# Kernel tuning notes

Measured on AMD Instinct MI355X. Metric: run time of the kernel, lower is better.

Reference implementation:

```python
import jax, jax.numpy as jnp
import numpy as np

N = 8192
D = 512
N_SLICE = 64
K = 8
H = 30 * K  # 240


def _gen_k_slice(rng):
    xx = rng.normal(0.0, 1.0, (N_SLICE, K, D))
    slices = np.zeros((N_SLICE, K, D), dtype=np.float64)
    for i in range(N_SLICE):
        _, _, vh = np.linalg.svd(xx[i], full_matrices=False)
        slices[i] = vh
    return slices.astype(np.float32)


def setup_inputs() -> dict:
    key = jax.random.key(0)
    k1, k2, k3, k4, k5, k6, k7 = jax.random.split(key, 7)
    rng = np.random.default_rng(0)
    # conv weights: PyTorch Conv1d default init ~ U(-s, s), s = 1/sqrt(fan_in)
    s1 = 1.0 / np.sqrt(K)
    s3 = 1.0 / np.sqrt(H)
    return {
        "X": jax.random.normal(k1, (N, D), dtype=jnp.float32),
        "Y": jax.random.normal(k2, (N, D), dtype=jnp.float32),
        "X_noise": jax.random.normal(k3, (N, N_SLICE * K), dtype=jnp.float32),
        "thetas": jnp.asarray(_gen_k_slice(rng)),                     # [S, K, D]
        "W1": jax.random.uniform(k4, (N_SLICE, H, K), jnp.float32, -s1, s1),
        "b1": jax.random.uniform(k5, (N_SLICE, H), jnp.float32, -s1, s1),
        "W3": jax.random.uniform(k6, (N_SLICE, H), jnp.float32, -s3, s3),
        "b3": jax.random.uniform(k7, (N_SLICE,), jnp.float32, -s3, s3),
        "sigma_noise": 0,
    }


def _mlp(sample, W1, b1, W3, b3):
    # sample: [N, S, K] -> grouped 1x1 conv k->H, relu, grouped conv H->1
    h1 = jax.nn.relu(jnp.einsum('nsk,shk->nsh', sample, W1) + b1[None])
    return jnp.einsum('nsh,sh->ns', h1, W3) + b3[None]  # [N, S]


def reference(X, Y, X_noise, thetas, W1, b1, W3, b3, sigma_noise):
    # batched per-slice projections (fuses the n_slice matmul loop)
    x_sample = jnp.einsum('nd,skd->nsk', X, thetas)  # [N, S, K]
    y_sample = jnp.einsum('nd,skd->nsk', Y, thetas)
    if sigma_noise > 0:
        x_sample = x_sample + sigma_noise * X_noise.reshape(X.shape[0], N_SLICE, K)
    pred_x = _mlp(x_sample, W1, b1, W3, b3)  # [N, S]
    pred_y = _mlp(y_sample, W1, b1, W3, b3)
    n_y = pred_y.shape[0]
    ret = jnp.mean(pred_x, axis=0) - jax.nn.logsumexp(
        pred_y - jnp.log(jnp.float32(n_y)), axis=0)
    return jnp.mean(-ret)
```

## Files before the change

kernel.cpp:

```cpp
#include <hip/hip_runtime.h>
#include <hip/hip_bf16.h>

#define NROWS 8192
#define DDIM  512
#define NS    64
#define KK    8
#define HH    240
#define SP2   72

typedef __attribute__((ext_vector_type(8))) _Float16 f16x8;
typedef __attribute__((ext_vector_type(4))) _Float16 f16x4;
typedef __attribute__((ext_vector_type(4))) float f32x4;
typedef __attribute__((ext_vector_type(2))) float f32x2;

typedef __attribute__((address_space(3))) void       lds_void;
typedef const __attribute__((address_space(1))) void gbl_cvoid;

__device__ inline unsigned pk2u(float a, float b) {
    auto h = __builtin_amdgcn_cvt_pkrtz(a, b);
    unsigned u;
    __builtin_memcpy(&u, &h, sizeof(u));
    return u;
}

__device__ inline void gl16(const ushort* g, ushort* l) {
    __builtin_amdgcn_global_load_lds((gbl_cvoid*)g, (lds_void*)l, 16, 0, 0);
}

#define XN (NROWS * DDIM)
__global__ __launch_bounds__(256)
void pack_kernel(const float* __restrict__ X, const float* __restrict__ Y,
                 const float* __restrict__ Th, const float* __restrict__ W1,
                 ushort* __restrict__ Xh, ushort* __restrict__ Yh,
                 ushort* __restrict__ Thh, ushort* __restrict__ W1h)
{
    int i = (blockIdx.x * 256 + threadIdx.x) * 4;
    const float* src; ushort* dst; int off;
    if (i < XN)               { src = X;  dst = Xh;  off = i; }
    else if (i < 2 * XN)      { src = Y;  dst = Yh;  off = i - XN; }
    else if (i < 2 * XN + 262144) { src = Th; dst = Thh; off = i - 2 * XN; }
    else                      { src = W1; dst = W1h; off = i - (2 * XN + 262144); }
    float4 v = *(const float4*)(src + off);
    *(uint2*)(dst + off) = make_uint2(pk2u(v.x, v.y), pk2u(v.z, v.w));
}

__global__ __launch_bounds__(256, 4)
void proj_mlp_kernel(const ushort* __restrict__ Xh,
                     const ushort* __restrict__ Yh,
                     const float* __restrict__ Xn,
                     const ushort* __restrict__ Thh,
                     const ushort* __restrict__ W1h,
                     const float* __restrict__ b1,
                     const float* __restrict__ W3,
                     const float* __restrict__ sig_p,
                     float* __restrict__ sumx,
                     float* __restrict__ maxy,
                     float* __restrict__ sey)
{
    __shared__ __align__(16) ushort smem[8192];
    ushort* sl = smem;

    const int tid  = threadIdx.x;
    const int w    = __builtin_amdgcn_readfirstlane(tid >> 6);
    const int lane = tid & 63;
    const int bx   = blockIdx.x;
    const int by   = blockIdx.y;

    const bool isX = (bx < 128);
    const int  bxl = isX ? bx : (bx - 128);
    const ushort* srcA = (isX ? Xh : Yh) + (size_t)bxl * 64 * DDIM;

    const int grow = (w << 4) + (lane >> 2);
    const int gchk = (lane & 3) ^ ((grow >> 1) & 3);
    const ushort* gA = srcA + (size_t)grow * DDIM + gchk * 8;
    const ushort* gB = Thh + (size_t)(by * 64 + grow) * DDIM + gchk * 8;
    const int woff = w * 512;

    f32x4 acc[2][2];
#pragma unroll
    for (int m = 0; m < 2; ++m)
#pragma unroll
        for (int n = 0; n < 2; ++n) acc[m][n] = (f32x4){0.f, 0.f, 0.f, 0.f};

    const int wr  = (w >> 1) * 32;
    const int wc  = (w & 1) * 32;
    const int r16 = lane & 15;
    const int hi4 = lane >> 4;

    int offA[2], offB[2];
#pragma unroll
    for (int m = 0; m < 2; ++m) {
        int row = wr + m * 16 + r16;
        offA[m] = row * 32 + ((hi4 ^ ((row >> 1) & 3)) * 8);
    }
#pragma unroll
    for (int n = 0; n < 2; ++n) {
        int row = wc + n * 16 + r16;
        offB[n] = 2048 + row * 32 + ((hi4 ^ ((row >> 1) & 3)) * 8);
    }

    gl16(gA, &smem[woff]);
    gl16(gB, &smem[2048 + woff]);
    __syncthreads();

#pragma unroll
    for (int kt = 0; kt < 16; ++kt) {
        const int cur = (kt & 1) * 4096;
        if (kt < 15) {
            const int nxt = 4096 - cur;
            gl16(gA + (kt + 1) * 32, &smem[nxt + woff]);
            gl16(gB + (kt + 1) * 32, &smem[nxt + 2048 + woff]);
        }
        f16x8 af[2], bfv[2];
#pragma unroll
        for (int m = 0; m < 2; ++m) af[m]  = *(const f16x8*)(smem + cur + offA[m]);
#pragma unroll
        for (int n = 0; n < 2; ++n) bfv[n] = *(const f16x8*)(smem + cur + offB[n]);
#pragma unroll
        for (int m = 0; m < 2; ++m)
#pragma unroll
            for (int n = 0; n < 2; ++n)
                acc[m][n] = __builtin_amdgcn_mfma_f32_16x16x32_f16(
                    af[m], bfv[n], acc[m][n], 0, 0, 0);
        __syncthreads();
    }

    const float sig = *sig_p;
    const bool addnoise = (sig > 0.f) && isX;
    const int n0g = bxl * 64;

#pragma unroll
    for (int m = 0; m < 2; ++m)
#pragma unroll
        for (int n = 0; n < 2; ++n) {
            const int col  = wc + n * 16 + r16;
            const int rowb = wr + m * 16 + hi4 * 4;
            float v[4];
#pragma unroll
            for (int j = 0; j < 4; ++j) {
                v[j] = acc[m][n][j];
                if (addnoise)
                    v[j] = fmaf(sig, Xn[(size_t)(n0g + rowb + j) * (NS * KK) + by * 64 + col], v[j]);
            }
            unsigned u01 = pk2u(v[0], v[1]);
            unsigned u23 = pk2u(v[2], v[3]);
            sl[(rowb + 0) * SP2 + col] = (ushort)u01;
            sl[(rowb + 1) * SP2 + col] = (ushort)(u01 >> 16);
            sl[(rowb + 2) * SP2 + col] = (ushort)u23;
            sl[(rowb + 3) * SP2 + col] = (ushort)(u23 >> 16);
        }
    __syncthreads();

#pragma unroll 1
    for (int si = 0; si < 2; ++si) {
        const int sloc = w * 2 + si;
        const int s    = by * 8 + sloc;

        f16x4 bsamp[4];
#pragma unroll
        for (int nt = 0; nt < 4; ++nt) {
            f16x4 t = {0, 0, 0, 0};
            if (hi4 < 2)
                t = *(const f16x4*)(sl + (nt * 16 + r16) * SP2 + sloc * 8 + hi4 * 4);
            bsamp[nt] = t;
        }

        const ushort* w1p = W1h + (size_t)s * HH * KK;
        const float*  b1p = b1 + s * HH;
        const float*  w3p = W3 + s * HH;

        f32x2 pn2[4];
#pragma unroll
        for (int nt = 0; nt < 4; ++nt) pn2[nt] = (f32x2){0.f, 0.f};

#pragma unroll 5
        for (int ht = 0; ht < HH / 16; ++ht) {
            f16x4 aw = {0, 0, 0, 0};
            if (hi4 < 2)
                aw = *(const f16x4*)(w1p + (ht * 16 + r16) * 8 + hi4 * 4);
            float4 b4 = *(const float4*)(b1p + ht * 16 + hi4 * 4);
            float4 w4 = *(const float4*)(w3p + ht * 16 + hi4 * 4);
            f32x4 z   = (f32x4){b4.x, b4.y, b4.z, b4.w};
            f32x2 w01 = (f32x2){w4.x, w4.y};
            f32x2 w23 = (f32x2){w4.z, w4.w};
            const f32x2 zero2 = (f32x2){0.f, 0.f};
#pragma unroll
            for (int nt = 0; nt < 4; ++nt) {
                f32x4 t = __builtin_amdgcn_mfma_f32_16x16x16f16(aw, bsamp[nt], z, 0, 0, 0);
                f32x2 t01 = (f32x2){t[0], t[1]};
                f32x2 t23 = (f32x2){t[2], t[3]};
                t01 = __builtin_elementwise_max(t01, zero2);
                t23 = __builtin_elementwise_max(t23, zero2);
                pn2[nt] = __builtin_elementwise_fma(t01, w01, pn2[nt]);
                pn2[nt] = __builtin_elementwise_fma(t23, w23, pn2[nt]);
            }
        }

        if (isX) {
            float lsum = 0.f;
#pragma unroll
            for (int nt = 0; nt < 4; ++nt) lsum += pn2[nt].x + pn2[nt].y;
#pragma unroll
            for (int off = 1; off < 64; off <<= 1)
                lsum += __shfl_xor(lsum, off);
            if (lane == 0) sumx[s * 128 + bxl] = lsum;
        } else {
            float p[4];
#pragma unroll
            for (int nt = 0; nt < 4; ++nt) {
                f32x2 v = pn2[nt];
                v.x += __shfl_xor(v.x, 16);
                v.y += __shfl_xor(v.y, 16);
                v.x += __shfl_xor(v.x, 32);
                v.y += __shfl_xor(v.y, 32);
                p[nt] = v.x + v.y;
            }
            float M = fmaxf(fmaxf(p[0], p[1]), fmaxf(p[2], p[3]));
            float se = __expf(p[0] - M) + __expf(p[1] - M)
                     + __expf(p[2] - M) + __expf(p[3] - M);
#pragma unroll
            for (int off = 1; off < 16; off <<= 1) {
                float Mo = __shfl_xor(M, off);
                float so = __shfl_xor(se, off);
                float Mm = fmaxf(M, Mo);
                se = se * __expf(M - Mm) + so * __expf(Mo - Mm);
                M = Mm;
            }
            if (lane == 0) {
                maxy[s * 128 + bxl] = M;
                sey[s * 128 + bxl]  = se;
            }
        }
    }
}

__global__ __launch_bounds__(256)
void final_kernel(const float* __restrict__ sumx,
                  const float* __restrict__ maxy,
                  const float* __restrict__ sey,
                  float* __restrict__ out)
{
    __shared__ float term_s[NS];
    const int tid = threadIdx.x;
    const int s = tid >> 2, q = tid & 3;
    const int base = s * 128 + q * 32;

    float sum = 0.f, M = -3.4e38f;
#pragma unroll 8
    for (int i = 0; i < 32; ++i) {
        sum += sumx[base + i];
        M = fmaxf(M, maxy[base + i]);
    }
    float se = 0.f;
#pragma unroll 8
    for (int i = 0; i < 32; ++i)
        se += sey[base + i] * __expf(maxy[base + i] - M);

#pragma unroll
    for (int off = 1; off < 4; off <<= 1) {
        float Mo = __shfl_xor(M, off);
        float so = __shfl_xor(se, off);
        float su = __shfl_xor(sum, off);
        float Mm = fmaxf(M, Mo);
        se = se * __expf(M - Mm) + so * __expf(Mo - Mm);
        M = Mm;
        sum += su;
    }
    if (q == 0)
        term_s[s] = M + logf(se) - logf((float)NROWS) - sum * (1.0f / (float)NROWS);
    __syncthreads();
    if (tid < 64) {
        float v = term_s[tid];
#pragma unroll
        for (int off = 1; off < 64; off <<= 1) v += __shfl_xor(v, off);
        if (tid == 0) out[0] = v * (1.0f / (float)NS);
    }
}

extern "C" void kernel_launch(void* const* d_in, const int* in_sizes, int n_in,
                              void* d_out, int out_size, void* d_ws, size_t ws_size,
                              hipStream_t stream)
{
    const float* X   = (const float*)d_in[0];
    const float* Y   = (const float*)d_in[1];
    const float* Xn  = (const float*)d_in[2];
    const float* Th  = (const float*)d_in[3];
    const float* W1  = (const float*)d_in[4];
    const float* b1  = (const float*)d_in[5];
    const float* W3  = (const float*)d_in[6];
    const float* sig = (const float*)d_in[8];

    ushort* Xh   = (ushort*)d_ws;
    ushort* Yh   = Xh + XN;
    ushort* Thh  = Yh + XN;
    ushort* W1h  = Thh + 262144;
    float*  sumx = (float*)(W1h + 122880);
    float*  maxy = sumx + NS * 128;
    float*  sey  = maxy + NS * 128;

    pack_kernel<<<(2 * XN + 262144 + 122880) / 1024, 256, 0, stream>>>(
        X, Y, Th, W1, Xh, Yh, Thh, W1h);

    dim3 g1(256, 8, 1);
    proj_mlp_kernel<<<g1, 256, 0, stream>>>(Xh, Yh, Xn, Thh, W1h, b1, W3,
                                            sig, sumx, maxy, sey);
    final_kernel<<<1, 256, 0, stream>>>(sumx, maxy, sey, (float*)d_out);
}
```

Measured before the change: 67.32 us.

## Process X and Y row tiles in the same block to share theta tiles and MLP weights

Each block now projects both an X tile and the matching Y tile against the same theta tile, then runs the per-slice MLP on both, so the grid is halved. The theta tile staged in LDS and the W1/b1/W3 loads are reused for two inputs, which cuts global and LDS traffic per output. In exchange each block uses more registers and LDS (two accumulator sets, a three-region staging buffer) and there are half as many blocks, which may lower occupancy and latency hiding.

Result: slower. 182.5 us (+171.1%).

```diff
diff --git a/kernel.cpp b/kernel.cpp
--- a/kernel.cpp
+++ b/kernel.cpp
@@ -7,6 +7,8 @@
 #define KK    8
 #define HH    240
 #define SP2   72
+#define RGN   2048
+#define STG   6144
 
 typedef __attribute__((ext_vector_type(8))) _Float16 f16x8;
 typedef __attribute__((ext_vector_type(4))) _Float16 f16x4;
@@ -57,30 +59,30 @@
                      float* __restrict__ maxy,
                      float* __restrict__ sey)
 {
-    __shared__ __align__(16) ushort smem[8192];
+    __shared__ __align__(16) ushort smem[2 * STG];
     ushort* sl = smem;
 
     const int tid  = threadIdx.x;
     const int w    = __builtin_amdgcn_readfirstlane(tid >> 6);
     const int lane = tid & 63;
-    const int bx   = blockIdx.x;
+    const int bxl  = blockIdx.x;
     const int by   = blockIdx.y;
-
-    const bool isX = (bx < 128);
-    const int  bxl = isX ? bx : (bx - 128);
-    const ushort* srcA = (isX ? Xh : Yh) + (size_t)bxl * 64 * DDIM;
 
     const int grow = (w << 4) + (lane >> 2);
     const int gchk = (lane & 3) ^ ((grow >> 1) & 3);
-    const ushort* gA = srcA + (size_t)grow * DDIM + gchk * 8;
-    const ushort* gB = Thh + (size_t)(by * 64 + grow) * DDIM + gchk * 8;
+    const ushort* gAX = Xh + (size_t)(bxl * 64 + grow) * DDIM + gchk * 8;
+    const ushort* gAY = Yh + (size_t)(bxl * 64 + grow) * DDIM + gchk * 8;
+    const ushort* gB  = Thh + (size_t)(by * 64 + grow) * DDIM + gchk * 8;
     const int woff = w * 512;
 
-    f32x4 acc[2][2];
+    f32x4 accX[2][2], accY[2][2];
 #pragma unroll
     for (int m = 0; m < 2; ++m)
 #pragma unroll
-        for (int n = 0; n < 2; ++n) acc[m][n] = (f32x4){0.f, 0.f, 0.f, 0.f};
+        for (int n = 0; n < 2; ++n) {
+            accX[m][n] = (f32x4){0.f, 0.f, 0.f, 0.f};
+            accY[m][n] = (f32x4){0.f, 0.f, 0.f, 0.f};
+        }
 
     const int wr  = (w >> 1) * 32;
     const int wc  = (w & 1) * 32;
@@ -96,37 +98,46 @@
 #pragma unroll
     for (int n = 0; n < 2; ++n) {
         int row = wc + n * 16 + r16;
-        offB[n] = 2048 + row * 32 + ((hi4 ^ ((row >> 1) & 3)) * 8);
-    }
-
-    gl16(gA, &smem[woff]);
-    gl16(gB, &smem[2048 + woff]);
+        offB[n] = 2 * RGN + row * 32 + ((hi4 ^ ((row >> 1) & 3)) * 8);
+    }
+
+    gl16(gAX, &smem[woff]);
+    gl16(gAY, &smem[RGN + woff]);
+    gl16(gB,  &smem[2 * RGN + woff]);
     __syncthreads();
 
 #pragma unroll
     for (int kt = 0; kt < 16; ++kt) {
-        const int cur = (kt & 1) * 4096;
+        const int cur = (kt & 1) * STG;
         if (kt < 15) {
-            const int nxt = 4096 - cur;
-            gl16(gA + (kt + 1) * 32, &smem[nxt + woff]);
-            gl16(gB + (kt + 1) * 32, &smem[nxt + 2048 + woff]);
-        }
-        f16x8 af[2], bfv[2];
-#pragma unroll
-        for (int m = 0; m < 2; ++m) af[m]  = *(const f16x8*)(smem + cur + offA[m]);
+            const int nxt = STG - cur;
+            const int k1 = (kt + 1) * 32;
+            gl16(gAX + k1, &smem[nxt + woff]);
+            gl16(gAY + k1, &smem[nxt + RGN + woff]);
+            gl16(gB  + k1, &smem[nxt + 2 * RGN + woff]);
+        }
+        f16x8 bfv[2], ax[2], ay[2];
 #pragma unroll
         for (int n = 0; n < 2; ++n) bfv[n] = *(const f16x8*)(smem + cur + offB[n]);
 #pragma unroll
+        for (int m = 0; m < 2; ++m) {
+            ax[m] = *(const f16x8*)(smem + cur + offA[m]);
+            ay[m] = *(const f16x8*)(smem + cur + RGN + offA[m]);
+        }
+#pragma unroll
         for (int m = 0; m < 2; ++m)
 #pragma unroll
-            for (int n = 0; n < 2; ++n)
-                acc[m][n] = __builtin_amdgcn_mfma_f32_16x16x32_f16(
-                    af[m], bfv[n], acc[m][n], 0, 0, 0);
+            for (int n = 0; n < 2; ++n) {
+                accX[m][n] = __builtin_amdgcn_mfma_f32_16x16x32_f16(
+                    ax[m], bfv[n], accX[m][n], 0, 0, 0);
+                accY[m][n] = __builtin_amdgcn_mfma_f32_16x16x32_f16(
+                    ay[m], bfv[n], accY[m][n], 0, 0, 0);
+            }
         __syncthreads();
     }
 
     const float sig = *sig_p;
-    const bool addnoise = (sig > 0.f) && isX;
+    const bool addnoise = (sig > 0.f);
     const int n0g = bxl * 64;
 
 #pragma unroll
@@ -135,19 +146,24 @@
         for (int n = 0; n < 2; ++n) {
             const int col  = wc + n * 16 + r16;
             const int rowb = wr + m * 16 + hi4 * 4;
-            float v[4];
+            float vx[4], vy[4];
 #pragma unroll
             for (int j = 0; j < 4; ++j) {
-                v[j] = acc[m][n][j];
+                vx[j] = accX[m][n][j];
                 if (addnoise)
-                    v[j] = fmaf(sig, Xn[(size_t)(n0g + rowb + j) * (NS * KK) + by * 64 + col], v[j]);
+                    vx[j] = fmaf(sig, Xn[(size_t)(n0g + rowb + j) * (NS * KK) + by * 64 + col], vx[j]);
+                vy[j] = accY[m][n][j];
             }
-            unsigned u01 = pk2u(v[0], v[1]);
-            unsigned u23 = pk2u(v[2], v[3]);
-            sl[(rowb + 0) * SP2 + col] = (ushort)u01;
-            sl[(rowb + 1) * SP2 + col] = (ushort)(u01 >> 16);
-            sl[(rowb + 2) * SP2 + col] = (ushort)u23;
-            sl[(rowb + 3) * SP2 + col] = (ushort)(u23 >> 16);
+            unsigned x01 = pk2u(vx[0], vx[1]), x23 = pk2u(vx[2], vx[3]);
+            unsigned y01 = pk2u(vy[0], vy[1]), y23 = pk2u(vy[2], vy[3]);
+            sl[(rowb + 0) * SP2 + col] = (ushort)x01;
+            sl[(rowb + 1) * SP2 + col] = (ushort)(x01 >> 16);
+            sl[(rowb + 2) * SP2 + col] = (ushort)x23;
+            sl[(rowb + 3) * SP2 + col] = (ushort)(x23 >> 16);
+            sl[(64 + rowb + 0) * SP2 + col] = (ushort)y01;
+            sl[(64 + rowb + 1) * SP2 + col] = (ushort)(y01 >> 16);
+            sl[(64 + rowb + 2) * SP2 + col] = (ushort)y23;
+            sl[(64 + rowb + 3) * SP2 + col] = (ushort)(y23 >> 16);
         }
     __syncthreads();
 
@@ -156,22 +172,27 @@
         const int sloc = w * 2 + si;
         const int s    = by * 8 + sloc;
 
-        f16x4 bsamp[4];
+        f16x4 bsx[4], bsy[4];
 #pragma unroll
         for (int nt = 0; nt < 4; ++nt) {
-            f16x4 t = {0, 0, 0, 0};
-            if (hi4 < 2)
-                t = *(const f16x4*)(sl + (nt * 16 + r16) * SP2 + sloc * 8 + hi4 * 4);
-            bsamp[nt] = t;
+            f16x4 tx = {0, 0, 0, 0}, ty = {0, 0, 0, 0};
+            if (hi4 < 2) {
+                tx = *(const f16x4*)(sl + (nt * 16 + r16) * SP2 + sloc * 8 + hi4 * 4);
+                ty = *(const f16x4*)(sl + (64 + nt * 16 + r16) * SP2 + sloc * 8 + hi4 * 4);
+            }
+            bsx[nt] = tx; bsy[nt] = ty;
         }
 
         const ushort* w1p = W1h + (size_t)s * HH * KK;
         const float*  b1p = b1 + s * HH;
         const float*  w3p = W3 + s * HH;
 
-        f32x2 pn2[4];
-#pragma unroll
-        for (int nt = 0; nt < 4; ++nt) pn2[nt] = (f32x2){0.f, 0.f};
+        f32x2 px2[4], py2[4];
+#pragma unroll
+        for (int nt = 0; nt < 4; ++nt) {
+            px2[nt] = (f32x2){0.f, 0.f};
+            py2[nt] = (f32x2){0.f, 0.f};
+        }
 
 #pragma unroll 5
         for (int ht = 0; ht < HH / 16; ++ht) {
@@ -186,50 +207,53 @@
             const f32x2 zero2 = (f32x2){0.f, 0.f};
 #pragma unroll
             for (int nt = 0; nt < 4; ++nt) {
-                f32x4 t = __builtin_amdgcn_mfma_f32_16x16x16f16(aw, bsamp[nt], z, 0, 0, 0);
-                f32x2 t01 = (f32x2){t[0], t[1]};
-                f32x2 t23 = (f32x2){t[2], t[3]};
-                t01 = __builtin_elementwise_max(t01, zero2);
-                t23 = __builtin_elementwise_max(t23, zero2);
-                pn2[nt] = __builtin_elementwise_fma(t01, w01, pn2[nt]);
-                pn2[nt] = __builtin_elementwise_fma(t23, w23, pn2[nt]);
+                f32x4 tx = __builtin_amdgcn_mfma_f32_16x16x16f16(aw, bsx[nt], z, 0, 0, 0);
+                f32x4 ty = __builtin_amdgcn_mfma_f32_16x16x16f16(aw, bsy[nt], z, 0, 0, 0);
+                f32x2 a01 = (f32x2){tx[0], tx[1]}, a23 = (f32x2){tx[2], tx[3]};
+                f32x2 c01 = (f32x2){ty[0], ty[1]}, c23 = (f32x2){ty[2], ty[3]};
+                a01 = __builtin_elementwise_max(a01, zero2);
+                a23 = __builtin_elementwise_max(a23, zero2);
+                c01 = __builtin_elementwise_max(c01, zero2);
+                c23 = __builtin_elementwise_max(c23, zero2);
+                px2[nt] = __builtin_elementwise_fma(a01, w01, px2[nt]);
+                px2[nt] = __builtin_elementwise_fma(a23, w23, px2[nt]);
+                py2[nt] = __builtin_elementwise_fma(c01, w01, py2[nt]);
+                py2[nt] = __builtin_elementwise_fma(c23, w23, py2[nt]);
             }
         }
 
-        if (isX) {
-            float lsum = 0.f;
-#pragma unroll
-            for (int nt = 0; nt < 4; ++nt) lsum += pn2[nt].x + pn2[nt].y;
-#pragma unroll
-            for (int off = 1; off < 64; off <<= 1)
-                lsum += __shfl_xor(lsum, off);
-            if (lane == 0) sumx[s * 128 + bxl] = lsum;
-        } else {
-            float p[4];
-#pragma unroll
-            for (int nt = 0; nt < 4; ++nt) {
-                f32x2 v = pn2[nt];
-                v.x += __shfl_xor(v.x, 16);
-                v.y += __shfl_xor(v.y, 16);
-                v.x += __shfl_xor(v.x, 32);
-                v.y += __shfl_xor(v.y, 32);
-                p[nt] = v.x + v.y;
-            }
-            float M = fmaxf(fmaxf(p[0], p[1]), fmaxf(p[2], p[3]));
-            float se = __expf(p[0] - M) + __expf(p[1] - M)
-                     + __expf(p[2] - M) + __expf(p[3] - M);
-#pragma unroll
-            for (int off = 1; off < 16; off <<= 1) {
-                float Mo = __shfl_xor(M, off);
-                float so = __shfl_xor(se, off);
-                float Mm = fmaxf(M, Mo);
-                se = se * __expf(M - Mm) + so * __expf(Mo - Mm);
-                M = Mm;
-            }
-            if (lane == 0) {
-                maxy[s * 128 + bxl] = M;
-                sey[s * 128 + bxl]  = se;
-            }
+        float lsum = 0.f;
+#pragma unroll
+        for (int nt = 0; nt < 4; ++nt) lsum += px2[nt].x + px2[nt].y;
+#pragma unroll
+        for (int off = 1; off < 64; off <<= 1)
+            lsum += __shfl_xor(lsum, off);
+        if (lane == 0) sumx[s * 128 + bxl] = lsum;
+
+        float p[4];
+#pragma unroll
+        for (int nt = 0; nt < 4; ++nt) {
+            f32x2 v = py2[nt];
+            v.x += __shfl_xor(v.x, 16);
+            v.y += __shfl_xor(v.y, 16);
+            v.x += __shfl_xor(v.x, 32);
+            v.y += __shfl_xor(v.y, 32);
+            p[nt] = v.x + v.y;
+        }
+        float M = fmaxf(fmaxf(p[0], p[1]), fmaxf(p[2], p[3]));
+        float se = __expf(p[0] - M) + __expf(p[1] - M)
+                 + __expf(p[2] - M) + __expf(p[3] - M);
+#pragma unroll
+        for (int off = 1; off < 16; off <<= 1) {
+            float Mo = __shfl_xor(M, off);
+            float so = __shfl_xor(se, off);
+            float Mm = fmaxf(M, Mo);
+            se = se * __expf(M - Mm) + so * __expf(Mo - Mm);
+            M = Mm;
+        }
+        if (lane == 0) {
+            maxy[s * 128 + bxl] = M;
+            sey[s * 128 + bxl]  = se;
         }
     }
 }
@@ -301,7 +325,7 @@
     pack_kernel<<<(2 * XN + 262144 + 122880) / 1024, 256, 0, stream>>>(
         X, Y, Th, W1, Xh, Yh, Thh, W1h);
 
-    dim3 g1(256, 8, 1);
+    dim3 g1(128, 8, 1);
     proj_mlp_kernel<<<g1, 256, 0, stream>>>(Xh, Yh, Xn, Thh, W1h, b1, W3,
                                             sig, sumx, maxy, sey);
     final_kernel<<<1, 256, 0, stream>>>(sumx, maxy, sey, (float*)d_out);
```
